# Optimization experiments

Hardware: AMD Instinct MI355X
Metric: run time of the kernel (lower is better)

## Reference

```python
import jax, jax.numpy as jnp
import numpy as np

H = 8      # num_attention_heads
DH = 96    # attention_head_size
LN_EPS = 1e-5


def setup_inputs() -> dict:
    key = jax.random.key(0)
    ks = jax.random.split(key, 12)
    B, S, D = 2, 768, 768
    sc = 0.02
    return {
        "hidden_states": jax.random.normal(ks[0], (B, S, D), jnp.float32),
        "distance_matrix": jax.random.uniform(ks[1], (B, S, S), jnp.float32) * 20.0,
        "angle_matrix": jax.random.uniform(ks[2], (B, S, S), jnp.float32) * np.pi,
        "attention_mask": jnp.ones((B, S), jnp.float32),
        "Wq": jax.random.normal(ks[3], (D, D), jnp.float32) * sc,
        "bq": jnp.zeros((D,), jnp.float32),
        "Wk": jax.random.normal(ks[4], (D, D), jnp.float32) * sc,
        "bk": jnp.zeros((D,), jnp.float32),
        "Wv": jax.random.normal(ks[5], (D, D), jnp.float32) * sc,
        "bv": jnp.zeros((D,), jnp.float32),
        "Wd": jax.random.normal(ks[6], (DH,), jnp.float32) * sc,
        "bd": jnp.zeros((DH,), jnp.float32),
        "Wa": jax.random.normal(ks[7], (DH,), jnp.float32) * sc,
        "ba": jnp.zeros((DH,), jnp.float32),
        "Wo": jax.random.normal(ks[8], (D, D), jnp.float32) * sc,
        "bo": jnp.zeros((D,), jnp.float32),
        "ln_g": jnp.ones((D,), jnp.float32),
        "ln_b": jnp.zeros((D,), jnp.float32),
    }


def _heads(x, B, S):
    # [B,S,D] -> [B,H,S,DH]
    return x.reshape(B, S, H, DH).transpose(0, 2, 1, 3)


def reference(hidden_states, distance_matrix, angle_matrix, attention_mask,
              Wq, bq, Wk, bk, Wv, bv, Wd, bd, Wa, ba, Wo, bo, ln_g, ln_b):
    B, S, D = hidden_states.shape
    q = _heads(hidden_states @ Wq.T + bq, B, S)   # [B,H,S,DH]
    k = _heads(hidden_states @ Wk.T + bk, B, S)
    v = _heads(hidden_states @ Wv.T + bv, B, S)

    scores = jnp.einsum('bhid,bhjd->bhij', q, k) / jnp.sqrt(jnp.float32(DH))

    # distance / angle relative-position biases: emb[b,i,j,:] = dist[b,i,j]*Wd + bd
    dist_emb = distance_matrix[..., None] * Wd + bd   # [B,S,S,DH]
    scores = scores + jnp.einsum('bhid,bijd->bhij', q, dist_emb)
    ang_emb = angle_matrix[..., None] * Wa + ba       # [B,S,S,DH]
    scores = scores + jnp.einsum('bhid,bijd->bhij', q, ang_emb)

    # key mask, broadcast over heads and query positions
    scores = scores + (1.0 - attention_mask)[:, None, None, :] * -10000.0

    probs = jax.nn.softmax(scores, axis=-1)           # [B,H,S,S]
    ctx = jnp.einsum('bhij,bhjd->bhid', probs, v)
    ctx = ctx.transpose(0, 2, 1, 3).reshape(B, S, D)  # [B,S,D]

    out = ctx @ Wo.T + bo
    x = out + hidden_states
    mu = jnp.mean(x, axis=-1, keepdims=True)
    var = jnp.var(x, axis=-1, keepdims=True)
    out = (x - mu) * jax.lax.rsqrt(var + LN_EPS) * ln_g + ln_b
    return out, probs
```

## Files before the change

### kernel.cpp

```cpp
#include <hip/hip_runtime.h>

#define B_  2
#define S_  768
#define D_  768
#define H_  8
#define DH_ 96

typedef unsigned short ushort_t;
typedef __bf16 bf16x8 __attribute__((ext_vector_type(8)));
typedef float  f32x4  __attribute__((ext_vector_type(4)));

__device__ inline ushort_t f2bf(float f) {
    union { float f; unsigned int u; } v; v.f = f;
    unsigned int u = v.u;
    unsigned int r = u + 0x7fffu + ((u >> 16) & 1u);
    return (ushort_t)(r >> 16);
}
__device__ inline float bf2f(ushort_t u) {
    union { unsigned int i; float f; } c; c.i = ((unsigned int)u) << 16;
    return c.f;
}

__global__ __launch_bounds__(256) void k_convert(
        const float* __restrict__ X, const float* __restrict__ Wq,
        const float* __restrict__ Wk, const float* __restrict__ Wv,
        const float* __restrict__ Wo,
        ushort_t* __restrict__ Xb, ushort_t* __restrict__ Wb) {
    const int NX4 = (B_ * S_ * D_) / 4;
    const int NW4 = (D_ * D_) / 4;
    int i = blockIdx.x * blockDim.x + threadIdx.x;
    float4 v;
    ushort_t* dst;
    if (i < NX4) {
        v = ((const float4*)X)[i];
        dst = Xb + i * 4;
    } else {
        int wi = i - NX4;
        int sel = wi / NW4;
        int off = wi - sel * NW4;
        const float* src = (sel == 0) ? Wq : (sel == 1) ? Wk : (sel == 2) ? Wv : Wo;
        v = ((const float4*)src)[off];
        dst = Wb + wi * 4;
    }
    ushort4 o;
    o.x = f2bf(v.x); o.y = f2bf(v.y); o.z = f2bf(v.z); o.w = f2bf(v.w);
    *(ushort4*)dst = o;
}

__device__ inline void gemm_bf16_64x64(
        const ushort_t* __restrict__ A, int lda,
        const ushort_t* __restrict__ Bt, int ldb, int maxBr,
        int K, int m0, int n0,
        ushort_t* As, ushort_t* Bs, f32x4 acc[2][2]) {
    const int tid  = threadIdx.x;
    const int lane = tid & 63, wave = tid >> 6;
    const int wm = (wave >> 1) * 32, wn = (wave & 1) * 32;
    const int lr = tid >> 2, lc = (tid & 3) * 8;
    const int fr = lane & 15, fk = (lane >> 4) * 8;
    int br = n0 + lr; if (br > maxBr) br = maxBr;
    const ushort_t* Arow = A + (size_t)(m0 + lr) * lda + lc;
    const ushort_t* Brow = Bt + (size_t)br * ldb + lc;
    for (int kt = 0; kt < K; kt += 32) {
        if (kt) __syncthreads();
        *(uint4*)&As[lr * 48 + lc] = *(const uint4*)(Arow + kt);
        *(uint4*)&Bs[lr * 48 + lc] = *(const uint4*)(Brow + kt);
        __syncthreads();
        bf16x8 a0 = *(const bf16x8*)&As[(wm      + fr) * 48 + fk];
        bf16x8 a1 = *(const bf16x8*)&As[(wm + 16 + fr) * 48 + fk];
        bf16x8 b0 = *(const bf16x8*)&Bs[(wn      + fr) * 48 + fk];
        bf16x8 b1 = *(const bf16x8*)&Bs[(wn + 16 + fr) * 48 + fk];
        acc[0][0] = __builtin_amdgcn_mfma_f32_16x16x32_bf16(a0, b0, acc[0][0], 0, 0, 0);
        acc[0][1] = __builtin_amdgcn_mfma_f32_16x16x32_bf16(a0, b1, acc[0][1], 0, 0, 0);
        acc[1][0] = __builtin_amdgcn_mfma_f32_16x16x32_bf16(a1, b0, acc[1][0], 0, 0, 0);
        acc[1][1] = __builtin_amdgcn_mfma_f32_16x16x32_bf16(a1, b1, acc[1][1], 0, 0, 0);
    }
}

__device__ inline void gemm_f32a_64x64(
        const float* __restrict__ A, int lda,
        const ushort_t* __restrict__ Bt, int ldb, int maxBr,
        int K, int m0, int n0,
        ushort_t* As, ushort_t* Bs, f32x4 acc[2][2]) {
    const int tid  = threadIdx.x;
    const int lane = tid & 63, wave = tid >> 6;
    const int wm = (wave >> 1) * 32, wn = (wave & 1) * 32;
    const int lr = tid >> 2, lc = (tid & 3) * 8;
    const int fr = lane & 15, fk = (lane >> 4) * 8;
    int br = n0 + lr; if (br > maxBr) br = maxBr;
    const float*    Arow = A  + (size_t)(m0 + lr) * lda + lc;
    const ushort_t* Brow = Bt + (size_t)br * ldb + lc;
    for (int kt = 0; kt < K; kt += 32) {
        if (kt) __syncthreads();
        float4 x0 = *(const float4*)(Arow + kt);
        float4 x1 = *(const float4*)(Arow + kt + 4);
        ushort4 o0, o1;
        o0.x = f2bf(x0.x); o0.y = f2bf(x0.y); o0.z = f2bf(x0.z); o0.w = f2bf(x0.w);
        o1.x = f2bf(x1.x); o1.y = f2bf(x1.y); o1.z = f2bf(x1.z); o1.w = f2bf(x1.w);
        *(ushort4*)&As[lr * 48 + lc]     = o0;
        *(ushort4*)&As[lr * 48 + lc + 4] = o1;
        *(uint4*)&Bs[lr * 48 + lc] = *(const uint4*)(Brow + kt);
        __syncthreads();
        bf16x8 a0 = *(const bf16x8*)&As[(wm      + fr) * 48 + fk];
        bf16x8 a1 = *(const bf16x8*)&As[(wm + 16 + fr) * 48 + fk];
        bf16x8 b0 = *(const bf16x8*)&Bs[(wn      + fr) * 48 + fk];
        bf16x8 b1 = *(const bf16x8*)&Bs[(wn + 16 + fr) * 48 + fk];
        acc[0][0] = __builtin_amdgcn_mfma_f32_16x16x32_bf16(a0, b0, acc[0][0], 0, 0, 0);
        acc[0][1] = __builtin_amdgcn_mfma_f32_16x16x32_bf16(a0, b1, acc[0][1], 0, 0, 0);
        acc[1][0] = __builtin_amdgcn_mfma_f32_16x16x32_bf16(a1, b0, acc[1][0], 0, 0, 0);
        acc[1][1] = __builtin_amdgcn_mfma_f32_16x16x32_bf16(a1, b1, acc[1][1], 0, 0, 0);
    }
}

__global__ __launch_bounds__(256) void k_qkv(
        const ushort_t* __restrict__ Xb, const ushort_t* __restrict__ Wb,
        const float* __restrict__ bq, const float* __restrict__ bk,
        const float* __restrict__ bv,
        ushort_t* __restrict__ Qb, ushort_t* __restrict__ Kb,
        ushort_t* __restrict__ Vtb) {
    __shared__ __align__(16) ushort_t As[64 * 48];
    __shared__ __align__(16) ushort_t Bs[64 * 48];
    f32x4 acc[2][2];
    #pragma unroll
    for (int i = 0; i < 2; i++)
        #pragma unroll
        for (int j = 0; j < 2; j++) acc[i][j] = (f32x4){0.f, 0.f, 0.f, 0.f};
    const int m0 = blockIdx.y * 64, n0 = blockIdx.x * 64;
    gemm_bf16_64x64(Xb, D_, Wb, D_, 3 * D_ - 1, D_, m0, n0, As, Bs, acc);
    const int lane = threadIdx.x & 63, wave = threadIdx.x >> 6;
    const int wm = (wave >> 1) * 32, wn = (wave & 1) * 32;
    #pragma unroll
    for (int ni = 0; ni < 2; ni++) {
        int gcol = n0 + wn + ni * 16 + (lane & 15);
        int g = gcol / D_, d768 = gcol - g * D_;
        int h = d768 / DH_, d = d768 - h * DH_;
        float bias = (g == 0 ? bq : (g == 1 ? bk : bv))[d768];
        #pragma unroll
        for (int mi = 0; mi < 2; mi++) {
            #pragma unroll
            for (int r = 0; r < 4; r++) {
                int grow = m0 + wm + mi * 16 + (lane >> 4) * 4 + r;
                int b = grow / S_, s = grow - b * S_;
                ushort_t ob = f2bf(acc[mi][ni][r] + bias);
                int bh = b * H_ + h;
                if (g == 0)      Qb[((size_t)bh * S_ + s) * DH_ + d] = ob;
                else if (g == 1) Kb[((size_t)bh * S_ + s) * DH_ + d] = ob;
                else             Vtb[((size_t)bh * DH_ + d) * S_ + s] = ob;
            }
        }
    }
}

__global__ __launch_bounds__(256) void k_qcoef(
        const ushort_t* __restrict__ Qb,
        const float* __restrict__ Wd, const float* __restrict__ bd,
        const float* __restrict__ Wa, const float* __restrict__ ba,
        float* __restrict__ qcoef) {
    const int wave = threadIdx.x >> 6, lane = threadIdx.x & 63;
    const int row = blockIdx.x * 4 + wave;
    const ushort_t* q = Qb + (size_t)row * DH_;
    float e0 = bf2f(q[lane]);
    float c0 = e0 * Wd[lane];
    float c1 = e0 * Wa[lane];
    float c2 = e0 * (bd[lane] + ba[lane]);
    if (lane < 32) {
        int d = 64 + lane;
        float e1 = bf2f(q[d]);
        c0 += e1 * Wd[d];
        c1 += e1 * Wa[d];
        c2 += e1 * (bd[d] + ba[d]);
    }
    #pragma unroll
    for (int o = 32; o > 0; o >>= 1) {
        c0 += __shfl_down(c0, o);
        c1 += __shfl_down(c1, o);
        c2 += __shfl_down(c2, o);
    }
    if (lane == 0) {
        qcoef[row * 3 + 0] = c0;
        qcoef[row * 3 + 1] = c1;
        qcoef[row * 3 + 2] = c2;
    }
}

__global__ __launch_bounds__(256) void k_scores(
        const ushort_t* __restrict__ Qb, const ushort_t* __restrict__ Kb,
        const float* __restrict__ qcoef,
        const float* __restrict__ distm, const float* __restrict__ angm,
        const float* __restrict__ mask, float* __restrict__ probs) {
    __shared__ __align__(16) ushort_t As[64 * 48];
    __shared__ __align__(16) ushort_t Bs[64 * 48];
    f32x4 acc[2][2];
    #pragma unroll
    for (int i = 0; i < 2; i++)
        #pragma unroll
        for (int j = 0; j < 2; j++) acc[i][j] = (f32x4){0.f, 0.f, 0.f, 0.f};
    const int bh = blockIdx.z, b = bh >> 3;
    const ushort_t* A  = Qb + (size_t)bh * S_ * DH_;
    const ushort_t* Bt = Kb + (size_t)bh * S_ * DH_;
    const int m0 = blockIdx.y * 64, n0 = blockIdx.x * 64;
    gemm_bf16_64x64(A, DH_, Bt, DH_, S_ - 1, DH_, m0, n0, As, Bs, acc);
    const int lane = threadIdx.x & 63, wave = threadIdx.x >> 6;
    const int wm = (wave >> 1) * 32, wn = (wave & 1) * 32;
    const float isq = 0.10206207261596577f;
    #pragma unroll
    for (int ni = 0; ni < 2; ni++) {
        int j = n0 + wn + ni * 16 + (lane & 15);
        float mb = (1.0f - mask[b * S_ + j]) * -10000.0f;
        #pragma unroll
        for (int mi = 0; mi < 2; mi++) {
            #pragma unroll
            for (int r = 0; r < 4; r++) {
                int i = m0 + wm + mi * 16 + (lane >> 4) * 4 + r;
                const float* qc = qcoef + ((size_t)bh * S_ + i) * 3;
                float dist = distm[((size_t)b * S_ + i) * S_ + j];
                float ang  = angm [((size_t)b * S_ + i) * S_ + j];
                float sres = acc[mi][ni][r] * isq + dist * qc[0] + ang * qc[1] + qc[2] + mb;
                probs[((size_t)bh * S_ + i) * S_ + j] = sres;
            }
        }
    }
}

__global__ __launch_bounds__(256) void k_softmax(float* __restrict__ probs) {
    float* p = probs + ((size_t)blockIdx.y * S_ + blockIdx.x) * S_;
    const int t = threadIdx.x;
    float v0 = p[t], v1 = p[t + 256], v2 = p[t + 512];
    __shared__ float rmax[4], rsum[4];
    float mx = fmaxf(v0, fmaxf(v1, v2));
    #pragma unroll
    for (int o = 32; o > 0; o >>= 1) mx = fmaxf(mx, __shfl_down(mx, o));
    if ((t & 63) == 0) rmax[t >> 6] = mx;
    __syncthreads();
    float m4 = fmaxf(fmaxf(rmax[0], rmax[1]), fmaxf(rmax[2], rmax[3]));
    float e0 = __expf(v0 - m4), e1 = __expf(v1 - m4), e2 = __expf(v2 - m4);
    float s = e0 + e1 + e2;
    #pragma unroll
    for (int o = 32; o > 0; o >>= 1) s += __shfl_down(s, o);
    if ((t & 63) == 0) rsum[t >> 6] = s;
    __syncthreads();
    float tot = rsum[0] + rsum[1] + rsum[2] + rsum[3];
    float inv = 1.0f / tot;
    p[t] = e0 * inv; p[t + 256] = e1 * inv; p[t + 512] = e2 * inv;
}

__global__ __launch_bounds__(256) void k_ctx(
        const float* __restrict__ probs, const ushort_t* __restrict__ Vtb,
        ushort_t* __restrict__ Ctxb) {
    __shared__ __align__(16) ushort_t As[64 * 48];
    __shared__ __align__(16) ushort_t Bs[64 * 48];
    f32x4 acc[2][2];
    #pragma unroll
    for (int i = 0; i < 2; i++)
        #pragma unroll
        for (int j = 0; j < 2; j++) acc[i][j] = (f32x4){0.f, 0.f, 0.f, 0.f};
    const int bh = blockIdx.z, b = bh >> 3, h = bh & 7;
    const float*    A  = probs + (size_t)bh * S_ * S_;
    const ushort_t* Bt = Vtb + (size_t)bh * DH_ * S_;
    const int m0 = blockIdx.y * 64, n0 = blockIdx.x * 64;
    gemm_f32a_64x64(A, S_, Bt, S_, DH_ - 1, S_, m0, n0, As, Bs, acc);
    const int lane = threadIdx.x & 63, wave = threadIdx.x >> 6;
    const int wm = (wave >> 1) * 32, wn = (wave & 1) * 32;
    #pragma unroll
    for (int ni = 0; ni < 2; ni++) {
        int gcol = n0 + wn + ni * 16 + (lane & 15);
        if (gcol >= DH_) continue;
        #pragma unroll
        for (int mi = 0; mi < 2; mi++) {
            #pragma unroll
            for (int r = 0; r < 4; r++) {
                int i = m0 + wm + mi * 16 + (lane >> 4) * 4 + r;
                Ctxb[((size_t)(b * S_ + i)) * D_ + h * DH_ + gcol] = f2bf(acc[mi][ni][r]);
            }
        }
    }
}

__global__ __launch_bounds__(256) void k_out(
        const ushort_t* __restrict__ Ctxb, const ushort_t* __restrict__ Wob,
        const float* __restrict__ bo, const float* __restrict__ hidden,
        float* __restrict__ xbuf) {
    __shared__ __align__(16) ushort_t As[64 * 48];
    __shared__ __align__(16) ushort_t Bs[64 * 48];
    f32x4 acc[2][2];
    #pragma unroll
    for (int i = 0; i < 2; i++)
        #pragma unroll
        for (int j = 0; j < 2; j++) acc[i][j] = (f32x4){0.f, 0.f, 0.f, 0.f};
    const int m0 = blockIdx.y * 64, n0 = blockIdx.x * 64;
    gemm_bf16_64x64(Ctxb, D_, Wob, D_, D_ - 1, D_, m0, n0, As, Bs, acc);
    const int lane = threadIdx.x & 63, wave = threadIdx.x >> 6;
    const int wm = (wave >> 1) * 32, wn = (wave & 1) * 32;
    #pragma unroll
    for (int ni = 0; ni < 2; ni++) {
        int gcol = n0 + wn + ni * 16 + (lane & 15);
        float bias = bo[gcol];
        #pragma unroll
        for (int mi = 0; mi < 2; mi++) {
            #pragma unroll
            for (int r = 0; r < 4; r++) {
                int grow = m0 + wm + mi * 16 + (lane >> 4) * 4 + r;
                float val = acc[mi][ni][r] + bias + hidden[(size_t)grow * D_ + gcol];
                xbuf[(size_t)grow * D_ + gcol] = val;
            }
        }
    }
}

__global__ __launch_bounds__(256) void k_ln(
        const float* __restrict__ xbuf, const float* __restrict__ g,
        const float* __restrict__ bb, float* __restrict__ out) {
    const float* x = xbuf + (size_t)blockIdx.x * D_;
    const int t = threadIdx.x;
    float a0 = x[t], a1 = x[t + 256], a2 = x[t + 512];
    float s = a0 + a1 + a2;
    float ss = a0 * a0 + a1 * a1 + a2 * a2;
    __shared__ float r1[4], r2[4];
    #pragma unroll
    for (int o = 32; o > 0; o >>= 1) { s += __shfl_down(s, o); ss += __shfl_down(ss, o); }
    if ((t & 63) == 0) { r1[t >> 6] = s; r2[t >> 6] = ss; }
    __syncthreads();
    float ts = r1[0] + r1[1] + r1[2] + r1[3];
    float tss = r2[0] + r2[1] + r2[2] + r2[3];
    float mu = ts * (1.0f / D_);
    float var = tss * (1.0f / D_) - mu * mu;
    float rstd = rsqrtf(var + 1e-5f);
    float* o = out + (size_t)blockIdx.x * D_;
    o[t]       = (a0 - mu) * rstd * g[t]       + bb[t];
    o[t + 256] = (a1 - mu) * rstd * g[t + 256] + bb[t + 256];
    o[t + 512] = (a2 - mu) * rstd * g[t + 512] + bb[t + 512];
}

extern "C" void kernel_launch(void* const* d_in, const int* in_sizes, int n_in,
                              void* d_out, int out_size, void* d_ws, size_t ws_size,
                              hipStream_t stream) {
    const float* X     = (const float*)d_in[0];
    const float* distm = (const float*)d_in[1];
    const float* angm  = (const float*)d_in[2];
    const float* mask  = (const float*)d_in[3];
    const float* Wq    = (const float*)d_in[4];
    const float* bq    = (const float*)d_in[5];
    const float* Wk    = (const float*)d_in[6];
    const float* bk    = (const float*)d_in[7];
    const float* Wv    = (const float*)d_in[8];
    const float* bv    = (const float*)d_in[9];
    const float* Wd    = (const float*)d_in[10];
    const float* bd    = (const float*)d_in[11];
    const float* Wa    = (const float*)d_in[12];
    const float* ba    = (const float*)d_in[13];
    const float* Wo    = (const float*)d_in[14];
    const float* bo    = (const float*)d_in[15];
    const float* ln_g  = (const float*)d_in[16];
    const float* ln_b  = (const float*)d_in[17];

    float* outp  = (float*)d_out;
    float* probs = (float*)d_out + (size_t)B_ * S_ * D_;

    char* ws = (char*)d_ws;
    ushort_t* Xb    = (ushort_t*)(ws + 0);
    ushort_t* Wb    = (ushort_t*)(ws + 2359296);
    ushort_t* Qb    = (ushort_t*)(ws + 7077888);
    ushort_t* Kb    = (ushort_t*)(ws + 9437184);
    ushort_t* Vtb   = (ushort_t*)(ws + 11796480);
    ushort_t* Ctxb  = (ushort_t*)(ws + 14155776);
    float*    qcoef = (float*)   (ws + 16515072);
    float*    xbuf  = (float*)   (ws + 16662528);

    k_convert<<<3456, 256, 0, stream>>>(X, Wq, Wk, Wv, Wo, Xb, Wb);
    k_qkv<<<dim3(36, 24), 256, 0, stream>>>(Xb, Wb, bq, bk, bv, Qb, Kb, Vtb);
    k_qcoef<<<3072, 256, 0, stream>>>(Qb, Wd, bd, Wa, ba, qcoef);
    k_scores<<<dim3(12, 12, 16), 256, 0, stream>>>(Qb, Kb, qcoef, distm, angm, mask, probs);
    k_softmax<<<dim3(768, 16), 256, 0, stream>>>(probs);
    k_ctx<<<dim3(2, 12, 16), 256, 0, stream>>>(probs, Vtb, Ctxb);
    k_out<<<dim3(12, 24), 256, 0, stream>>>(Ctxb, Wb + (size_t)2304 * 768, bo, X, xbuf);
    k_ln<<<1536, 256, 0, stream>>>(xbuf, ln_g, ln_b, outp);
}
```

Measured before the change: 200.6 us.

## Fuse softmax with PV GEMM, use direct global-to-LDS loads, enlarge QKV tile

Scores now go to a workspace buffer. A new fused kernel computes row max and sum, writes the normalized probs, and feeds bf16 exp values straight into the PV MFMA. This removes the separate softmax kernel and the fp32 probs re-read by the ctx GEMM. The GEMM staging is switched to global_load_lds 16-byte direct loads with an unpadded 32-wide LDS layout, which may cause bank conflicts. The QKV GEMM grows to a 128x64 tile so each block does more work per B load.

Result: slower. 206.7 us (+3.1%).

```diff
diff --git a/kernel.cpp b/kernel.cpp
--- a/kernel.cpp
+++ b/kernel.cpp
@@ -1,4 +1,5 @@
 #include <hip/hip_runtime.h>
+#include <stdint.h>
 
 #define B_  2
 #define S_  768
@@ -19,6 +20,14 @@
 __device__ inline float bf2f(ushort_t u) {
     union { unsigned int i; float f; } c; c.i = ((unsigned int)u) << 16;
     return c.f;
+}
+
+__device__ inline void glds16(const void* gp, void* lp) {
+    auto g = reinterpret_cast<const __attribute__((address_space(1))) uint32_t*>(
+        reinterpret_cast<uintptr_t>(gp));
+    auto l = reinterpret_cast<__attribute__((address_space(3))) uint32_t*>(
+        reinterpret_cast<uintptr_t>(lp));
+    __builtin_amdgcn_global_load_lds(g, l, 16, 0, 0);
 }
 
 __global__ __launch_bounds__(256) void k_convert(
@@ -47,63 +56,30 @@
     *(ushort4*)dst = o;
 }
 
-__device__ inline void gemm_bf16_64x64(
+__device__ inline void gemm64_glds(
         const ushort_t* __restrict__ A, int lda,
-        const ushort_t* __restrict__ Bt, int ldb, int maxBr,
+        const ushort_t* __restrict__ Bt, int ldb,
         int K, int m0, int n0,
         ushort_t* As, ushort_t* Bs, f32x4 acc[2][2]) {
     const int tid  = threadIdx.x;
     const int lane = tid & 63, wave = tid >> 6;
     const int wm = (wave >> 1) * 32, wn = (wave & 1) * 32;
-    const int lr = tid >> 2, lc = (tid & 3) * 8;
     const int fr = lane & 15, fk = (lane >> 4) * 8;
-    int br = n0 + lr; if (br > maxBr) br = maxBr;
-    const ushort_t* Arow = A + (size_t)(m0 + lr) * lda + lc;
-    const ushort_t* Brow = Bt + (size_t)br * ldb + lc;
+    const int sr = wave * 16 + (lane >> 2);
+    const int sc = (lane & 3) * 8;
+    const ushort_t* Ap = A  + (size_t)(m0 + sr) * lda + sc;
+    const ushort_t* Bp = Bt + (size_t)(n0 + sr) * ldb + sc;
+    ushort_t* AsW = As + wave * 512;
+    ushort_t* BsW = Bs + wave * 512;
     for (int kt = 0; kt < K; kt += 32) {
         if (kt) __syncthreads();
-        *(uint4*)&As[lr * 48 + lc] = *(const uint4*)(Arow + kt);
-        *(uint4*)&Bs[lr * 48 + lc] = *(const uint4*)(Brow + kt);
+        glds16(Ap + kt, AsW);
+        glds16(Bp + kt, BsW);
         __syncthreads();
-        bf16x8 a0 = *(const bf16x8*)&As[(wm      + fr) * 48 + fk];
-        bf16x8 a1 = *(const bf16x8*)&As[(wm + 16 + fr) * 48 + fk];
-        bf16x8 b0 = *(const bf16x8*)&Bs[(wn      + fr) * 48 + fk];
-        bf16x8 b1 = *(const bf16x8*)&Bs[(wn + 16 + fr) * 48 + fk];
-        acc[0][0] = __builtin_amdgcn_mfma_f32_16x16x32_bf16(a0, b0, acc[0][0], 0, 0, 0);
-        acc[0][1] = __builtin_amdgcn_mfma_f32_16x16x32_bf16(a0, b1, acc[0][1], 0, 0, 0);
-        acc[1][0] = __builtin_amdgcn_mfma_f32_16x16x32_bf16(a1, b0, acc[1][0], 0, 0, 0);
-        acc[1][1] = __builtin_amdgcn_mfma_f32_16x16x32_bf16(a1, b1, acc[1][1], 0, 0, 0);
-    }
-}
-
-__device__ inline void gemm_f32a_64x64(
-        const float* __restrict__ A, int lda,
-        const ushort_t* __restrict__ Bt, int ldb, int maxBr,
-        int K, int m0, int n0,
-        ushort_t* As, ushort_t* Bs, f32x4 acc[2][2]) {
-    const int tid  = threadIdx.x;
-    const int lane = tid & 63, wave = tid >> 6;
-    const int wm = (wave >> 1) * 32, wn = (wave & 1) * 32;
-    const int lr = tid >> 2, lc = (tid & 3) * 8;
-    const int fr = lane & 15, fk = (lane >> 4) * 8;
-    int br = n0 + lr; if (br > maxBr) br = maxBr;
-    const float*    Arow = A  + (size_t)(m0 + lr) * lda + lc;
-    const ushort_t* Brow = Bt + (size_t)br * ldb + lc;
-    for (int kt = 0; kt < K; kt += 32) {
-        if (kt) __syncthreads();
-        float4 x0 = *(const float4*)(Arow + kt);
-        float4 x1 = *(const float4*)(Arow + kt + 4);
-        ushort4 o0, o1;
-        o0.x = f2bf(x0.x); o0.y = f2bf(x0.y); o0.z = f2bf(x0.z); o0.w = f2bf(x0.w);
-        o1.x = f2bf(x1.x); o1.y = f2bf(x1.y); o1.z = f2bf(x1.z); o1.w = f2bf(x1.w);
-        *(ushort4*)&As[lr * 48 + lc]     = o0;
-        *(ushort4*)&As[lr * 48 + lc + 4] = o1;
-        *(uint4*)&Bs[lr * 48 + lc] = *(const uint4*)(Brow + kt);
-        __syncthreads();
-        bf16x8 a0 = *(const bf16x8*)&As[(wm      + fr) * 48 + fk];
-        bf16x8 a1 = *(const bf16x8*)&As[(wm + 16 + fr) * 48 + fk];
-        bf16x8 b0 = *(const bf16x8*)&Bs[(wn      + fr) * 48 + fk];
-        bf16x8 b1 = *(const bf16x8*)&Bs[(wn + 16 + fr) * 48 + fk];
+        bf16x8 a0 = *(const bf16x8*)&As[(wm      + fr) * 32 + fk];
+        bf16x8 a1 = *(const bf16x8*)&As[(wm + 16 + fr) * 32 + fk];
+        bf16x8 b0 = *(const bf16x8*)&Bs[(wn      + fr) * 32 + fk];
+        bf16x8 b1 = *(const bf16x8*)&Bs[(wn + 16 + fr) * 32 + fk];
         acc[0][0] = __builtin_amdgcn_mfma_f32_16x16x32_bf16(a0, b0, acc[0][0], 0, 0, 0);
         acc[0][1] = __builtin_amdgcn_mfma_f32_16x16x32_bf16(a0, b1, acc[0][1], 0, 0, 0);
         acc[1][0] = __builtin_amdgcn_mfma_f32_16x16x32_bf16(a1, b0, acc[1][0], 0, 0, 0);
@@ -117,31 +93,57 @@
         const float* __restrict__ bv,
         ushort_t* __restrict__ Qb, ushort_t* __restrict__ Kb,
         ushort_t* __restrict__ Vtb) {
-    __shared__ __align__(16) ushort_t As[64 * 48];
-    __shared__ __align__(16) ushort_t Bs[64 * 48];
-    f32x4 acc[2][2];
-    #pragma unroll
-    for (int i = 0; i < 2; i++)
+    __shared__ __align__(16) ushort_t As[128 * 32];
+    __shared__ __align__(16) ushort_t Bs[64 * 32];
+    f32x4 acc[4][2];
+    #pragma unroll
+    for (int i = 0; i < 4; i++)
         #pragma unroll
         for (int j = 0; j < 2; j++) acc[i][j] = (f32x4){0.f, 0.f, 0.f, 0.f};
-    const int m0 = blockIdx.y * 64, n0 = blockIdx.x * 64;
-    gemm_bf16_64x64(Xb, D_, Wb, D_, 3 * D_ - 1, D_, m0, n0, As, Bs, acc);
-    const int lane = threadIdx.x & 63, wave = threadIdx.x >> 6;
-    const int wm = (wave >> 1) * 32, wn = (wave & 1) * 32;
+    const int tid = threadIdx.x, lane = tid & 63, wave = tid >> 6;
+    const int m0 = blockIdx.y * 128, n0 = blockIdx.x * 64;
+    const int fr = lane & 15, fk = (lane >> 4) * 8;
+    const int wm = (wave >> 1) * 64, wn = (wave & 1) * 32;
+    const int sr = lane >> 2, sc = (lane & 3) * 8;
+    const ushort_t* Ap0 = Xb + (size_t)(m0 + wave * 32 + sr) * D_ + sc;
+    const ushort_t* Ap1 = Ap0 + 16 * D_;
+    const ushort_t* Bp  = Wb + (size_t)(n0 + wave * 16 + sr) * D_ + sc;
+    ushort_t* AsW0 = As + wave * 1024;
+    ushort_t* AsW1 = As + wave * 1024 + 512;
+    ushort_t* BsW  = Bs + wave * 512;
+    for (int kt = 0; kt < D_; kt += 32) {
+        if (kt) __syncthreads();
+        glds16(Ap0 + kt, AsW0);
+        glds16(Ap1 + kt, AsW1);
+        glds16(Bp  + kt, BsW);
+        __syncthreads();
+        bf16x8 a[4], b[2];
+        #pragma unroll
+        for (int mi = 0; mi < 4; mi++)
+            a[mi] = *(const bf16x8*)&As[(wm + mi * 16 + fr) * 32 + fk];
+        #pragma unroll
+        for (int ni = 0; ni < 2; ni++)
+            b[ni] = *(const bf16x8*)&Bs[(wn + ni * 16 + fr) * 32 + fk];
+        #pragma unroll
+        for (int mi = 0; mi < 4; mi++)
+            #pragma unroll
+            for (int ni = 0; ni < 2; ni++)
+                acc[mi][ni] = __builtin_amdgcn_mfma_f32_16x16x32_bf16(a[mi], b[ni], acc[mi][ni], 0, 0, 0);
+    }
     #pragma unroll
     for (int ni = 0; ni < 2; ni++) {
-        int gcol = n0 + wn + ni * 16 + (lane & 15);
+        int gcol = n0 + wn + ni * 16 + fr;
         int g = gcol / D_, d768 = gcol - g * D_;
         int h = d768 / DH_, d = d768 - h * DH_;
         float bias = (g == 0 ? bq : (g == 1 ? bk : bv))[d768];
         #pragma unroll
-        for (int mi = 0; mi < 2; mi++) {
+        for (int mi = 0; mi < 4; mi++) {
             #pragma unroll
             for (int r = 0; r < 4; r++) {
                 int grow = m0 + wm + mi * 16 + (lane >> 4) * 4 + r;
-                int b = grow / S_, s = grow - b * S_;
+                int bidx = grow / S_, s = grow - bidx * S_;
                 ushort_t ob = f2bf(acc[mi][ni][r] + bias);
-                int bh = b * H_ + h;
+                int bh = bidx * H_ + h;
                 if (g == 0)      Qb[((size_t)bh * S_ + s) * DH_ + d] = ob;
                 else if (g == 1) Kb[((size_t)bh * S_ + s) * DH_ + d] = ob;
                 else             Vtb[((size_t)bh * DH_ + d) * S_ + s] = ob;
@@ -186,9 +188,9 @@
         const ushort_t* __restrict__ Qb, const ushort_t* __restrict__ Kb,
         const float* __restrict__ qcoef,
         const float* __restrict__ distm, const float* __restrict__ angm,
-        const float* __restrict__ mask, float* __restrict__ probs) {
-    __shared__ __align__(16) ushort_t As[64 * 48];
-    __shared__ __align__(16) ushort_t Bs[64 * 48];
+        const float* __restrict__ mask, float* __restrict__ Sc) {
+    __shared__ __align__(16) ushort_t As[64 * 32];
+    __shared__ __align__(16) ushort_t Bs[64 * 32];
     f32x4 acc[2][2];
     #pragma unroll
     for (int i = 0; i < 2; i++)
@@ -198,7 +200,7 @@
     const ushort_t* A  = Qb + (size_t)bh * S_ * DH_;
     const ushort_t* Bt = Kb + (size_t)bh * S_ * DH_;
     const int m0 = blockIdx.y * 64, n0 = blockIdx.x * 64;
-    gemm_bf16_64x64(A, DH_, Bt, DH_, S_ - 1, DH_, m0, n0, As, Bs, acc);
+    gemm64_glds(A, DH_, Bt, DH_, DH_, m0, n0, As, Bs, acc);
     const int lane = threadIdx.x & 63, wave = threadIdx.x >> 6;
     const int wm = (wave >> 1) * 32, wn = (wave & 1) * 32;
     const float isq = 0.10206207261596577f;
@@ -214,63 +216,87 @@
                 const float* qc = qcoef + ((size_t)bh * S_ + i) * 3;
                 float dist = distm[((size_t)b * S_ + i) * S_ + j];
                 float ang  = angm [((size_t)b * S_ + i) * S_ + j];
-                float sres = acc[mi][ni][r] * isq + dist * qc[0] + ang * qc[1] + qc[2] + mb;
-                probs[((size_t)bh * S_ + i) * S_ + j] = sres;
+                Sc[((size_t)bh * S_ + i) * S_ + j] =
+                    acc[mi][ni][r] * isq + dist * qc[0] + ang * qc[1] + qc[2] + mb;
             }
         }
     }
 }
 
-__global__ __launch_bounds__(256) void k_softmax(float* __restrict__ probs) {
-    float* p = probs + ((size_t)blockIdx.y * S_ + blockIdx.x) * S_;
-    const int t = threadIdx.x;
-    float v0 = p[t], v1 = p[t + 256], v2 = p[t + 512];
-    __shared__ float rmax[4], rsum[4];
-    float mx = fmaxf(v0, fmaxf(v1, v2));
-    #pragma unroll
-    for (int o = 32; o > 0; o >>= 1) mx = fmaxf(mx, __shfl_down(mx, o));
-    if ((t & 63) == 0) rmax[t >> 6] = mx;
+__global__ __launch_bounds__(256) void k_attnctx(
+        const float* __restrict__ Sc, const ushort_t* __restrict__ Vtb,
+        float* __restrict__ probs, ushort_t* __restrict__ Ctxb) {
+    const int bh = blockIdx.y, b = bh >> 3, h = bh & 7;
+    const int r0 = blockIdx.x * 32;
+    const float* S = Sc + ((size_t)bh * S_ + r0) * S_;
+    const ushort_t* Vt = Vtb + (size_t)bh * DH_ * S_;
+    __shared__ float mrow[32], lrow[32];
+    __shared__ __align__(16) ushort_t Ps[32 * 32];
+    __shared__ __align__(16) ushort_t Vs[96 * 32];
+    const int tid = threadIdx.x, lane = tid & 63, wave = tid >> 6;
+    for (int rr = 0; rr < 8; rr++) {
+        int row = wave * 8 + rr;
+        const float* sr = S + (size_t)row * S_;
+        float4 x0 = ((const float4*)sr)[lane];
+        float4 x1 = ((const float4*)sr)[lane + 64];
+        float4 x2 = ((const float4*)sr)[lane + 128];
+        float mx = fmaxf(fmaxf(fmaxf(x0.x, x0.y), fmaxf(x0.z, x0.w)),
+                   fmaxf(fmaxf(fmaxf(x1.x, x1.y), fmaxf(x1.z, x1.w)),
+                         fmaxf(fmaxf(x2.x, x2.y), fmaxf(x2.z, x2.w))));
+        #pragma unroll
+        for (int o = 32; o > 0; o >>= 1) mx = fmaxf(mx, __shfl_down(mx, o));
+        mx = __shfl(mx, 0);
+        float s = __expf(x0.x - mx) + __expf(x0.y - mx) + __expf(x0.z - mx) + __expf(x0.w - mx)
+                + __expf(x1.x - mx) + __expf(x1.y - mx) + __expf(x1.z - mx) + __expf(x1.w - mx)
+                + __expf(x2.x - mx) + __expf(x2.y - mx) + __expf(x2.z - mx) + __expf(x2.w - mx);
+        #pragma unroll
+        for (int o = 32; o > 0; o >>= 1) s += __shfl_down(s, o);
+        if (lane == 0) { mrow[row] = mx; lrow[row] = s; }
+    }
     __syncthreads();
-    float m4 = fmaxf(fmaxf(rmax[0], rmax[1]), fmaxf(rmax[2], rmax[3]));
-    float e0 = __expf(v0 - m4), e1 = __expf(v1 - m4), e2 = __expf(v2 - m4);
-    float s = e0 + e1 + e2;
-    #pragma unroll
-    for (int o = 32; o > 0; o >>= 1) s += __shfl_down(s, o);
-    if ((t & 63) == 0) rsum[t >> 6] = s;
-    __syncthreads();
-    float tot = rsum[0] + rsum[1] + rsum[2] + rsum[3];
-    float inv = 1.0f / tot;
-    p[t] = e0 * inv; p[t + 256] = e1 * inv; p[t + 512] = e2 * inv;
-}
-
-__global__ __launch_bounds__(256) void k_ctx(
-        const float* __restrict__ probs, const ushort_t* __restrict__ Vtb,
-        ushort_t* __restrict__ Ctxb) {
-    __shared__ __align__(16) ushort_t As[64 * 48];
-    __shared__ __align__(16) ushort_t Bs[64 * 48];
-    f32x4 acc[2][2];
-    #pragma unroll
-    for (int i = 0; i < 2; i++)
-        #pragma unroll
-        for (int j = 0; j < 2; j++) acc[i][j] = (f32x4){0.f, 0.f, 0.f, 0.f};
-    const int bh = blockIdx.z, b = bh >> 3, h = bh & 7;
-    const float*    A  = probs + (size_t)bh * S_ * S_;
-    const ushort_t* Bt = Vtb + (size_t)bh * DH_ * S_;
-    const int m0 = blockIdx.y * 64, n0 = blockIdx.x * 64;
-    gemm_f32a_64x64(A, S_, Bt, S_, DH_ - 1, S_, m0, n0, As, Bs, acc);
-    const int lane = threadIdx.x & 63, wave = threadIdx.x >> 6;
-    const int wm = (wave >> 1) * 32, wn = (wave & 1) * 32;
-    #pragma unroll
-    for (int ni = 0; ni < 2; ni++) {
-        int gcol = n0 + wn + ni * 16 + (lane & 15);
-        if (gcol >= DH_) continue;
-        #pragma unroll
-        for (int mi = 0; mi < 2; mi++) {
-            #pragma unroll
-            for (int r = 0; r < 4; r++) {
-                int i = m0 + wm + mi * 16 + (lane >> 4) * 4 + r;
-                Ctxb[((size_t)(b * S_ + i)) * D_ + h * DH_ + gcol] = f2bf(acc[mi][ni][r]);
-            }
+    const int mrow0 = (wave & 1) * 16;
+    const int nb    = (wave >> 1) * 48;
+    const int fr = lane & 15, fk = (lane >> 4) * 8;
+    const int prow = tid >> 3, pc = (tid & 7) * 4;
+    const float pm = mrow[prow];
+    const float pinvl = 1.0f / lrow[prow];
+    f32x4 acc[3];
+    #pragma unroll
+    for (int i = 0; i < 3; i++) acc[i] = (f32x4){0.f, 0.f, 0.f, 0.f};
+    const int vr0 = tid >> 2, vc0 = (tid & 3) * 8;
+    const int i1 = tid + 256;
+    const int vr1 = i1 >> 2, vc1 = (i1 & 3) * 8;
+    for (int kt = 0; kt < S_; kt += 32) {
+        if (kt) __syncthreads();
+        {
+            float4 s4 = *(const float4*)(S + (size_t)prow * S_ + kt + pc);
+            float e0 = __expf(s4.x - pm), e1 = __expf(s4.y - pm);
+            float e2 = __expf(s4.z - pm), e3 = __expf(s4.w - pm);
+            ushort4 pb;
+            pb.x = f2bf(e0); pb.y = f2bf(e1); pb.z = f2bf(e2); pb.w = f2bf(e3);
+            *(ushort4*)&Ps[prow * 32 + pc] = pb;
+            float4 pn = {e0 * pinvl, e1 * pinvl, e2 * pinvl, e3 * pinvl};
+            *(float4*)&probs[((size_t)bh * S_ + r0 + prow) * S_ + kt + pc] = pn;
+        }
+        *(uint4*)&Vs[vr0 * 32 + vc0] = *(const uint4*)(Vt + (size_t)vr0 * S_ + kt + vc0);
+        if (i1 < 384)
+            *(uint4*)&Vs[vr1 * 32 + vc1] = *(const uint4*)(Vt + (size_t)vr1 * S_ + kt + vc1);
+        __syncthreads();
+        bf16x8 a = *(const bf16x8*)&Ps[(mrow0 + fr) * 32 + fk];
+        #pragma unroll
+        for (int ni = 0; ni < 3; ni++) {
+            bf16x8 bfr = *(const bf16x8*)&Vs[(nb + ni * 16 + fr) * 32 + fk];
+            acc[ni] = __builtin_amdgcn_mfma_f32_16x16x32_bf16(a, bfr, acc[ni], 0, 0, 0);
+        }
+    }
+    #pragma unroll
+    for (int ni = 0; ni < 3; ni++) {
+        int col = nb + ni * 16 + fr;
+        #pragma unroll
+        for (int r = 0; r < 4; r++) {
+            int row = mrow0 + (lane >> 4) * 4 + r;
+            float o = acc[ni][r] / lrow[row];
+            Ctxb[((size_t)(b * S_ + r0 + row)) * D_ + h * DH_ + col] = f2bf(o);
         }
     }
 }
@@ -279,15 +305,15 @@
         const ushort_t* __restrict__ Ctxb, const ushort_t* __restrict__ Wob,
         const float* __restrict__ bo, const float* __restrict__ hidden,
         float* __restrict__ xbuf) {
-    __shared__ __align__(16) ushort_t As[64 * 48];
-    __shared__ __align__(16) ushort_t Bs[64 * 48];
+    __shared__ __align__(16) ushort_t As[64 * 32];
+    __shared__ __align__(16) ushort_t Bs[64 * 32];
     f32x4 acc[2][2];
     #pragma unroll
     for (int i = 0; i < 2; i++)
         #pragma unroll
         for (int j = 0; j < 2; j++) acc[i][j] = (f32x4){0.f, 0.f, 0.f, 0.f};
     const int m0 = blockIdx.y * 64, n0 = blockIdx.x * 64;
-    gemm_bf16_64x64(Ctxb, D_, Wob, D_, D_ - 1, D_, m0, n0, As, Bs, acc);
+    gemm64_glds(Ctxb, D_, Wob, D_, D_, m0, n0, As, Bs, acc);
     const int lane = threadIdx.x & 63, wave = threadIdx.x >> 6;
     const int wm = (wave >> 1) * 32, wn = (wave & 1) * 32;
     #pragma unroll
@@ -299,8 +325,8 @@
             #pragma unroll
             for (int r = 0; r < 4; r++) {
                 int grow = m0 + wm + mi * 16 + (lane >> 4) * 4 + r;
-                float val = acc[mi][ni][r] + bias + hidden[(size_t)grow * D_ + gcol];
-                xbuf[(size_t)grow * D_ + gcol] = val;
+                xbuf[(size_t)grow * D_ + gcol] =
+                    acc[mi][ni][r] + bias + hidden[(size_t)grow * D_ + gcol];
             }
         }
     }
@@ -364,13 +390,13 @@
     ushort_t* Ctxb  = (ushort_t*)(ws + 14155776);
     float*    qcoef = (float*)   (ws + 16515072);
     float*    xbuf  = (float*)   (ws + 16662528);
+    float*    Sc    = (float*)   (ws + 21381120);
 
     k_convert<<<3456, 256, 0, stream>>>(X, Wq, Wk, Wv, Wo, Xb, Wb);
-    k_qkv<<<dim3(36, 24), 256, 0, stream>>>(Xb, Wb, bq, bk, bv, Qb, Kb, Vtb);
+    k_qkv<<<dim3(36, 12), 256, 0, stream>>>(Xb, Wb, bq, bk, bv, Qb, Kb, Vtb);
     k_qcoef<<<3072, 256, 0, stream>>>(Qb, Wd, bd, Wa, ba, qcoef);
-    k_scores<<<dim3(12, 12, 16), 256, 0, stream>>>(Qb, Kb, qcoef, distm, angm, mask, probs);
-    k_softmax<<<dim3(768, 16), 256, 0, stream>>>(probs);
-    k_ctx<<<dim3(2, 12, 16), 256, 0, stream>>>(probs, Vtb, Ctxb);
+    k_scores<<<dim3(12, 12, 16), 256, 0, stream>>>(Qb, Kb, qcoef, distm, angm, mask, Sc);
+    k_attnctx<<<dim3(24, 16), 256, 0, stream>>>(Sc, Vtb, probs, Ctxb);
     k_out<<<dim3(12, 24), 256, 0, stream>>>(Ctxb, Wb + (size_t)2304 * 768, bo, X, xbuf);
     k_ln<<<1536, 256, 0, stream>>>(xbuf, ln_g, ln_b, outp);
 }
```
